# Optimization experiments

Measured on AMD Instinct MI355X. Metric: run time of the kernel, lower is better.

Reference implementation:

```python
import jax, jax.numpy as jnp
import numpy as np
import math

LOG2PI = math.log(2.0 * math.pi)
ALPHA, BETA, GAMMA = 1.0, 4.0, 1.0  # coefficients (mi, tc, dw_kl)


def gaussian_log_density(samples, mean, log_var):
    inv_sigma = jnp.exp(-log_var)
    tmp = samples - mean
    return -0.5 * (tmp * tmp * inv_sigma + log_var + LOG2PI)


def log_importance_weight_matrix(batch_size, dataset_size):
    # Faithful port of the TF/beta-tcvae MSS importance weights.
    N = float(dataset_size)
    M = batch_size - 1
    strat_weight = (N - M) / (N * M)
    W = jnp.full((batch_size, batch_size), 1.0 / M, dtype=jnp.float32)
    W = W.at[:, 0].set(1.0 / N)
    W = W.at[:, 1].set(strat_weight)
    W = W.at[M - 1, 0].set(strat_weight)
    return jnp.log(W)


def setup_inputs() -> dict:
    key = jax.random.key(0)
    k1, k2, k3, k4, k5 = jax.random.split(key, 5)
    B, D, F = 2048, 16, 512
    return {
        "x": jax.random.normal(k1, (B, F), dtype=jnp.float32),
        "reconstruction": jax.random.normal(k2, (B, F), dtype=jnp.float32),
        "mu": jax.random.normal(k3, (B, D), dtype=jnp.float32),
        "log_var": jax.random.normal(k4, (B, D), dtype=jnp.float32) * 0.5,
        "z": jax.random.normal(k5, (B, D), dtype=jnp.float32),
        "size_dataset": 100000,
    }


def reference(x, reconstruction, mu, log_var, z, size_dataset):
    B = z.shape[0]
    # reconstruction loss: mean over batch of per-sample MAE == global mean abs error
    recon_loss = jnp.mean(jnp.abs(x - reconstruction))

    # log q(z|x): [B]
    log_q_zx = jnp.sum(gaussian_log_density(z, mu, log_var), axis=-1)

    # pairwise densities: [B, B, D]  (z_i under q(.|x_j))
    log_qz_prob = gaussian_log_density(z[:, None, :], mu[None, :, :], log_var[None, :, :])

    # log p(z): note the original passes ones_like(z) as log_var (faithful quirk)
    log_prior = jnp.sum(
        gaussian_log_density(z, jnp.zeros_like(z), jnp.ones_like(z)), axis=-1
    )

    # MSS importance weights [B, B]
    logiw = log_importance_weight_matrix(B, size_dataset)

    # log q(z): logsumexp over batch of joint densities + weights
    log_qz = jax.nn.logsumexp(jnp.sum(log_qz_prob, axis=2) + logiw, axis=1)  # [B]

    # log prod_d q(z_d): dimension-wise logsumexp then sum over dims
    log_qz_product = jnp.sum(
        jax.nn.logsumexp(log_qz_prob + logiw[:, :, None], axis=1), axis=1
    )  # [B]

    mutual_info_loss = jnp.mean(log_q_zx - log_qz)
    tc_loss = jnp.mean(log_qz - log_qz_product)
    dimension_wise_kl = jnp.mean(log_qz_product - log_prior)

    total_loss = (
        recon_loss
        + ALPHA * mutual_info_loss
        + BETA * tc_loss
        + GAMMA * dimension_wise_kl
    )
    return total_loss
```

## Files before the change

### kernel.cpp

```cpp
#include <hip/hip_runtime.h>
#include <math.h>

#define LOG2PI_F 1.8378770664093453f
#define LOG2E_F  1.4426950408889634f
#define LN2_F    0.6931471805599453f
#define EXP_NEG1 0.36787944117144233f

#define TI   16
#define JSP  8
#define STG  64
#define ROWF 52

__device__ __forceinline__ float exp2_(float x) { return __builtin_amdgcn_exp2f(x); }
__device__ __forceinline__ float log2_(float x) { return __builtin_amdgcn_logf(x); }


__global__ __launch_bounds__(256) void k_recon(const float4* __restrict__ x,
                                               const float4* __restrict__ r,
                                               float* __restrict__ acc, int n4) {
    float s = 0.0f;
    for (int idx = blockIdx.x * 256 + threadIdx.x; idx < n4; idx += gridDim.x * 256) {
        float4 a = x[idx], b = r[idx];
        s += fabsf(a.x - b.x) + fabsf(a.y - b.y) + fabsf(a.z - b.z) + fabsf(a.w - b.w);
    }
    #pragma unroll
    for (int off = 32; off > 0; off >>= 1) s += __shfl_down(s, off);
    __shared__ float red[4];
    int lane = threadIdx.x & 63, wv = threadIdx.x >> 6;
    if (lane == 0) red[wv] = s;
    __syncthreads();
    if (threadIdx.x == 0) atomicAdd(&acc[0], red[0] + red[1] + red[2] + red[3]);
}

__global__ __launch_bounds__(256) void k_prep(const float* __restrict__ mu,
                                              const float* __restrict__ lv,
                                              const float* __restrict__ z,
                                              const int* __restrict__ nds,
                                              float* __restrict__ AC,
                                              float* __restrict__ acc, int B) {
    int idx = blockIdx.x * 256 + threadIdx.x;
    int j = idx >> 4, d = idx & 15;
    float m = mu[idx], l = lv[idx], zz = z[idx];
    float is = __expf(-l);
    float a = -0.5f * LOG2E_F * is;
    float b = -2.0f * a * m;
    float ec = fmaf(-0.5f * LOG2E_F, l + LOG2PI_F, a * m * m);

    float Nf = (float)(*nds);
    float Mf = (float)(B - 1);
    float strat = (Nf - Mf) / (Nf * Mf);
    float w = (j == 0) ? (1.0f / Nf) : ((j == 1) ? strat : (1.0f / Mf));

    float* row = AC + (size_t)j * ROWF;
    row[d] = a;
    row[16 + d] = b;
    row[32 + d] = w * exp2_(ec);
    float es = ec;
    es += __shfl_xor(es, 1); es += __shfl_xor(es, 2);
    es += __shfl_xor(es, 4); es += __shfl_xor(es, 8);
    if (d == 0) row[48] = w * exp2_(es);

    float t = zz - m;
    float ga = -0.5f * (fmaf(t * t, is, l) + LOG2PI_F);
    float gb = -0.5f * (fmaf(zz * zz, EXP_NEG1, 1.0f) + LOG2PI_F);
    #pragma unroll
    for (int off = 32; off > 0; off >>= 1) { ga += __shfl_down(ga, off); gb += __shfl_down(gb, off); }
    __shared__ float ra[4], rb[4];
    int lane = threadIdx.x & 63, wv = threadIdx.x >> 6;
    if (lane == 0) { ra[wv] = ga; rb[wv] = gb; }
    __syncthreads();
    if (threadIdx.x == 0) {
        atomicAdd(&acc[1], ra[0] + ra[1] + ra[2] + ra[3]);
        atomicAdd(&acc[2], rb[0] + rb[1] + rb[2] + rb[3]);
    }
}

#define DIM(AQ, BQ, CQ, comp, dd, SACC) \
    e = fmaf(AQ.comp, v2[dd], BQ.comp * v[dd]); SACC += e; \
    sd[dd] = fmaf(CQ.comp, exp2_(e), sd[dd]);

__global__ __launch_bounds__(256) void k_pair(const float* __restrict__ AC,
                                              const float* __restrict__ z,
                                              float* __restrict__ Racc,
                                              int B, int jch) {
    __shared__ float sbuf[2][STG * ROWF];
    __shared__ float red[4][TI][17];

    const int il = threadIdx.x & 15;
    const int jg = threadIdx.x >> 4;
    const int i  = blockIdx.x * TI + il;
    const int jbase = blockIdx.y * jch;

    float v[16], v2[16];
    {
        const float4* zp = (const float4*)(z + (size_t)i * 16);
        float4 z0 = zp[0], z1 = zp[1], z2 = zp[2], z3 = zp[3];
        v[0]=z0.x; v[1]=z0.y; v[2]=z0.z; v[3]=z0.w;
        v[4]=z1.x; v[5]=z1.y; v[6]=z1.z; v[7]=z1.w;
        v[8]=z2.x; v[9]=z2.y; v[10]=z2.z; v[11]=z2.w;
        v[12]=z3.x; v[13]=z3.y; v[14]=z3.z; v[15]=z3.w;
        #pragma unroll
        for (int d = 0; d < 16; d++) v2[d] = v[d] * v[d];
    }

    float sd[16];
    #pragma unroll
    for (int d = 0; d < 16; d++) sd[d] = 0.0f;
    float stot = 0.0f;

    auto load_stage = [&](int buf, int st) {
        const float4* g = (const float4*)(AC + (size_t)(jbase + st * STG) * ROWF);
        float4* dst = (float4*)sbuf[buf];
        #pragma unroll
        for (int k = 0; k < 4; ++k) {
            int idx = threadIdx.x + k * 256;
            if (idx < (STG * ROWF) / 4) dst[idx] = g[idx];
        }
    };

    const int nst = jch / STG;
    load_stage(0, 0);
    __syncthreads();
    for (int st = 0; st < nst; ++st) {
        if (st + 1 < nst) load_stage((st + 1) & 1, st + 1);
        const float* base = sbuf[st & 1];
        #pragma unroll
        for (int k = 0; k < 4; ++k) {
            const float* rp = base + (jg + 16 * k) * ROWF;
            const float4* r4 = (const float4*)rp;
            float4 A0 = r4[0], A1 = r4[1], A2 = r4[2], A3 = r4[3];
            float4 Bv0 = r4[4], Bv1 = r4[5], Bv2 = r4[6], Bv3 = r4[7];
            float4 Cv0 = r4[8], Cv1 = r4[9], Cv2 = r4[10], Cv3 = r4[11];
            float  P = rp[48];
            float s2a = 0.0f, s2b = 0.0f, e;
            DIM(A0, Bv0, Cv0, x, 0, s2a)  DIM(A0, Bv0, Cv0, y, 1, s2b)
            DIM(A0, Bv0, Cv0, z, 2, s2a)  DIM(A0, Bv0, Cv0, w, 3, s2b)
            DIM(A1, Bv1, Cv1, x, 4, s2a)  DIM(A1, Bv1, Cv1, y, 5, s2b)
            DIM(A1, Bv1, Cv1, z, 6, s2a)  DIM(A1, Bv1, Cv1, w, 7, s2b)
            DIM(A2, Bv2, Cv2, x, 8, s2a)  DIM(A2, Bv2, Cv2, y, 9, s2b)
            DIM(A2, Bv2, Cv2, z, 10, s2a) DIM(A2, Bv2, Cv2, w, 11, s2b)
            DIM(A3, Bv3, Cv3, x, 12, s2a) DIM(A3, Bv3, Cv3, y, 13, s2b)
            DIM(A3, Bv3, Cv3, z, 14, s2a) DIM(A3, Bv3, Cv3, w, 15, s2b)
            stot = fmaf(P, exp2_(s2a + s2b), stot);
        }
        __syncthreads();
    }

    #pragma unroll
    for (int msk = 16; msk <= 32; msk <<= 1) {
        stot += __shfl_xor(stot, msk);
        #pragma unroll
        for (int d = 0; d < 16; d++) sd[d] += __shfl_xor(sd[d], msk);
    }
    int lane = threadIdx.x & 63, wv = threadIdx.x >> 6;
    if (lane < 16) {
        red[wv][lane][0] = stot;
        #pragma unroll
        for (int d = 0; d < 16; d++) red[wv][lane][1 + d] = sd[d];
    }
    __syncthreads();
    for (int t = threadIdx.x; t < TI * 17; t += 256) {
        int il2 = t / 17, c = t % 17;
        float s = red[0][il2][c] + red[1][il2][c] + red[2][il2][c] + red[3][il2][c];
        atomicAdd(&Racc[(size_t)(blockIdx.x * TI + il2) * 17 + c], s);
    }
}

__global__ __launch_bounds__(256) void k_logs(const float* __restrict__ Racc,
                                              const float* __restrict__ AC,
                                              const float* __restrict__ z,
                                              const int* __restrict__ nds,
                                              float* __restrict__ acc, int B) {
    int i = blockIdx.x * 256 + threadIdx.x;
    const float* R = Racc + (size_t)i * 17;
    float S = R[0];
    float Sd[16];
    #pragma unroll
    for (int d = 0; d < 16; d++) Sd[d] = R[1 + d];

    if (i == B - 2) {
        const float* row0 = AC;
        const float* vv = z + (size_t)i * 16;
        float Nf = (float)(*nds);
        float Mf = (float)(B - 1);
        float strat = (Nf - Mf) / (Nf * Mf);
        float dwN = (strat - 1.0f / Nf) * Nf;
        float s2 = 0.0f;
        #pragma unroll
        for (int d = 0; d < 16; d++) {
            float vd = vv[d];
            float e = fmaf(row0[d], vd * vd, row0[16 + d] * vd);
            s2 += e;
            Sd[d] += dwN * row0[32 + d] * exp2_(e);
        }
        S += dwN * row0[48] * exp2_(s2);
    }

    float lqz = log2_(S) * LN2_F;
    float lqzp = 0.0f;
    #pragma unroll
    for (int d = 0; d < 16; d++) lqzp += log2_(Sd[d]);
    lqzp *= LN2_F;

    #pragma unroll
    for (int off = 32; off > 0; off >>= 1) {
        lqz += __shfl_down(lqz, off);
        lqzp += __shfl_down(lqzp, off);
    }
    __shared__ float ra[4], rb[4];
    int lane = threadIdx.x & 63, wv = threadIdx.x >> 6;
    if (lane == 0) { ra[wv] = lqz; rb[wv] = lqzp; }
    __syncthreads();
    if (threadIdx.x == 0) {
        atomicAdd(&acc[3], ra[0] + ra[1] + ra[2] + ra[3]);
        atomicAdd(&acc[4], rb[0] + rb[1] + rb[2] + rb[3]);
    }
}

__global__ void k_final(const float* __restrict__ acc, float* __restrict__ out,
                        float invBF, float invB) {
    out[0] = acc[0] * invBF +
             (acc[1] + 3.0f * acc[3] - 3.0f * acc[4] - acc[2]) * invB;
}

extern "C" void kernel_launch(void* const* d_in, const int* in_sizes, int n_in,
                              void* d_out, int out_size, void* d_ws, size_t ws_size,
                              hipStream_t stream) {
    const float* x   = (const float*)d_in[0];
    const float* rec = (const float*)d_in[1];
    const float* mu  = (const float*)d_in[2];
    const float* lv  = (const float*)d_in[3];
    const float* z   = (const float*)d_in[4];
    const int*   nds = (const int*)d_in[5];

    const int BD = in_sizes[2];
    const int B  = BD / 16;
    const int BF = in_sizes[0];
    const int n4 = BF / 4;

    float* acc  = (float*)d_ws;
    float* Racc = acc + 8;
    float* AC   = Racc + (size_t)B * 17;

    hipMemsetAsync(d_ws, 0, (8 + (size_t)B * 17) * sizeof(float), stream);
    k_prep <<<BD / 256, 256, 0, stream>>>(mu, lv, z, nds, AC, acc, B);
    k_recon<<<512, 256, 0, stream>>>((const float4*)x, (const float4*)rec, acc, n4);
    dim3 gp(B / TI, JSP);
    k_pair <<<gp, 256, 0, stream>>>(AC, z, Racc, B, B / JSP);
    k_logs <<<B / 256, 256, 0, stream>>>(Racc, AC, z, nds, acc, B);
    k_final<<<1, 1, 0, stream>>>(acc, (float*)d_out, 1.0f / (float)BF, 1.0f / (float)B);
}
```

Measured before the change: 100.1 us.

## Fuse prep and recon kernels, register-block two rows per thread, drop atomics and memset

Merges the prep and reconstruction-loss kernels into one launch. Partial sums now go to per-block slots reduced by a multi-thread final kernel, which replaces the atomics and removes the workspace memset. The pair kernel now handles two z rows per thread (TI 32, JSP 16) so each shared-memory load of the coefficients is reused twice. It also loads its whole 128-row j chunk into shared memory once instead of double-buffering. The intent is fewer launches, less atomic contention and more ALU work per LDS read, at the cost of higher register pressure and a larger strided partial-sum buffer.

```diff
diff --git a/kernel.cpp b/kernel.cpp
--- a/kernel.cpp
+++ b/kernel.cpp
@@ -6,177 +6,192 @@
 #define LN2_F    0.6931471805599453f
 #define EXP_NEG1 0.36787944117144233f
 
-#define TI   16
-#define JSP  8
-#define STG  64
+#define TI   32
+#define JSP  16
+#define JCH  128
 #define ROWF 52
 
 __device__ __forceinline__ float exp2_(float x) { return __builtin_amdgcn_exp2f(x); }
 __device__ __forceinline__ float log2_(float x) { return __builtin_amdgcn_logf(x); }
 
 
-__global__ __launch_bounds__(256) void k_recon(const float4* __restrict__ x,
-                                               const float4* __restrict__ r,
-                                               float* __restrict__ acc, int n4) {
-    float s = 0.0f;
-    for (int idx = blockIdx.x * 256 + threadIdx.x; idx < n4; idx += gridDim.x * 256) {
-        float4 a = x[idx], b = r[idx];
-        s += fabsf(a.x - b.x) + fabsf(a.y - b.y) + fabsf(a.z - b.z) + fabsf(a.w - b.w);
-    }
-    #pragma unroll
-    for (int off = 32; off > 0; off >>= 1) s += __shfl_down(s, off);
-    __shared__ float red[4];
-    int lane = threadIdx.x & 63, wv = threadIdx.x >> 6;
-    if (lane == 0) red[wv] = s;
-    __syncthreads();
-    if (threadIdx.x == 0) atomicAdd(&acc[0], red[0] + red[1] + red[2] + red[3]);
-}
-
-__global__ __launch_bounds__(256) void k_prep(const float* __restrict__ mu,
-                                              const float* __restrict__ lv,
-                                              const float* __restrict__ z,
-                                              const int* __restrict__ nds,
-                                              float* __restrict__ AC,
-                                              float* __restrict__ acc, int B) {
-    int idx = blockIdx.x * 256 + threadIdx.x;
-    int j = idx >> 4, d = idx & 15;
-    float m = mu[idx], l = lv[idx], zz = z[idx];
-    float is = __expf(-l);
-    float a = -0.5f * LOG2E_F * is;
-    float b = -2.0f * a * m;
-    float ec = fmaf(-0.5f * LOG2E_F, l + LOG2PI_F, a * m * m);
-
-    float Nf = (float)(*nds);
-    float Mf = (float)(B - 1);
-    float strat = (Nf - Mf) / (Nf * Mf);
-    float w = (j == 0) ? (1.0f / Nf) : ((j == 1) ? strat : (1.0f / Mf));
-
-    float* row = AC + (size_t)j * ROWF;
-    row[d] = a;
-    row[16 + d] = b;
-    row[32 + d] = w * exp2_(ec);
-    float es = ec;
-    es += __shfl_xor(es, 1); es += __shfl_xor(es, 2);
-    es += __shfl_xor(es, 4); es += __shfl_xor(es, 8);
-    if (d == 0) row[48] = w * exp2_(es);
-
-    float t = zz - m;
-    float ga = -0.5f * (fmaf(t * t, is, l) + LOG2PI_F);
-    float gb = -0.5f * (fmaf(zz * zz, EXP_NEG1, 1.0f) + LOG2PI_F);
-    #pragma unroll
-    for (int off = 32; off > 0; off >>= 1) { ga += __shfl_down(ga, off); gb += __shfl_down(gb, off); }
+__global__ __launch_bounds__(256) void k_prep_recon(
+        const float* __restrict__ mu, const float* __restrict__ lv,
+        const float* __restrict__ z, const int* __restrict__ nds,
+        const float4* __restrict__ x, const float4* __restrict__ r,
+        float* __restrict__ AC, float* __restrict__ PPa, float* __restrict__ PPb,
+        float* __restrict__ RP, int B, int n4, int prepBlks) {
     __shared__ float ra[4], rb[4];
-    int lane = threadIdx.x & 63, wv = threadIdx.x >> 6;
-    if (lane == 0) { ra[wv] = ga; rb[wv] = gb; }
-    __syncthreads();
-    if (threadIdx.x == 0) {
-        atomicAdd(&acc[1], ra[0] + ra[1] + ra[2] + ra[3]);
-        atomicAdd(&acc[2], rb[0] + rb[1] + rb[2] + rb[3]);
-    }
-}
-
-#define DIM(AQ, BQ, CQ, comp, dd, SACC) \
-    e = fmaf(AQ.comp, v2[dd], BQ.comp * v[dd]); SACC += e; \
-    sd[dd] = fmaf(CQ.comp, exp2_(e), sd[dd]);
+    const int lane = threadIdx.x & 63, wv = threadIdx.x >> 6;
+
+    if ((int)blockIdx.x < prepBlks) {
+        int idx = blockIdx.x * 256 + threadIdx.x;
+        int j = idx >> 4, d = idx & 15;
+        float m = mu[idx], l = lv[idx], zz = z[idx];
+        float is = __expf(-l);
+        float a = -0.5f * LOG2E_F * is;
+        float b = -2.0f * a * m;
+        float ec = fmaf(-0.5f * LOG2E_F, l + LOG2PI_F, a * m * m);
+
+        float Nf = (float)(*nds);
+        float Mf = (float)(B - 1);
+        float strat = (Nf - Mf) / (Nf * Mf);
+        float w = (j == 0) ? (1.0f / Nf) : ((j == 1) ? strat : (1.0f / Mf));
+
+        float* row = AC + (size_t)j * ROWF;
+        row[d] = a;
+        row[16 + d] = b;
+        row[32 + d] = w * exp2_(ec);
+        float es = ec;
+        es += __shfl_xor(es, 1); es += __shfl_xor(es, 2);
+        es += __shfl_xor(es, 4); es += __shfl_xor(es, 8);
+        if (d == 0) row[48] = w * exp2_(es);
+
+        float t = zz - m;
+        float ga = -0.5f * (fmaf(t * t, is, l) + LOG2PI_F);
+        float gb = -0.5f * (fmaf(zz * zz, EXP_NEG1, 1.0f) + LOG2PI_F);
+        #pragma unroll
+        for (int off = 32; off > 0; off >>= 1) { ga += __shfl_down(ga, off); gb += __shfl_down(gb, off); }
+        if (lane == 0) { ra[wv] = ga; rb[wv] = gb; }
+        __syncthreads();
+        if (threadIdx.x == 0) {
+            PPa[blockIdx.x] = ra[0] + ra[1] + ra[2] + ra[3];
+            PPb[blockIdx.x] = rb[0] + rb[1] + rb[2] + rb[3];
+        }
+    } else {
+        int bid = blockIdx.x - prepBlks;
+        float s = 0.0f;
+        for (int idx = bid * 256 + threadIdx.x; idx < n4; idx += 512 * 256) {
+            float4 a = x[idx], b = r[idx];
+            s += fabsf(a.x - b.x) + fabsf(a.y - b.y) + fabsf(a.z - b.z) + fabsf(a.w - b.w);
+        }
+        #pragma unroll
+        for (int off = 32; off > 0; off >>= 1) s += __shfl_down(s, off);
+        if (lane == 0) ra[wv] = s;
+        __syncthreads();
+        if (threadIdx.x == 0) RP[bid] = ra[0] + ra[1] + ra[2] + ra[3];
+    }
+}
+
+#define DIM2(AQ, BQ, CQ, comp, dd, SA, SB) \
+    e = fmaf(AQ.comp, va2[dd], BQ.comp * va[dd]); SA += e; sda[dd] = fmaf(CQ.comp, exp2_(e), sda[dd]); \
+    e = fmaf(AQ.comp, vb2[dd], BQ.comp * vb[dd]); SB += e; sdb[dd] = fmaf(CQ.comp, exp2_(e), sdb[dd]);
 
 __global__ __launch_bounds__(256) void k_pair(const float* __restrict__ AC,
                                               const float* __restrict__ z,
-                                              float* __restrict__ Racc,
+                                              float* __restrict__ Rs,
                                               int B, int jch) {
-    __shared__ float sbuf[2][STG * ROWF];
+    __shared__ float sbuf[JCH * ROWF];
     __shared__ float red[4][TI][17];
 
     const int il = threadIdx.x & 15;
     const int jg = threadIdx.x >> 4;
-    const int i  = blockIdx.x * TI + il;
+    const int i0 = blockIdx.x * TI + il;
     const int jbase = blockIdx.y * jch;
 
-    float v[16], v2[16];
     {
-        const float4* zp = (const float4*)(z + (size_t)i * 16);
+        const float4* g = (const float4*)(AC + (size_t)jbase * ROWF);
+        float4* dst = (float4*)sbuf;
+        #pragma unroll
+        for (int k = 0; k < 7; ++k) {
+            int idx = threadIdx.x + k * 256;
+            if (idx < (JCH * ROWF) / 4) dst[idx] = g[idx];
+        }
+    }
+
+    float va[16], va2[16], vb[16], vb2[16];
+    {
+        const float4* zp = (const float4*)(z + (size_t)i0 * 16);
         float4 z0 = zp[0], z1 = zp[1], z2 = zp[2], z3 = zp[3];
-        v[0]=z0.x; v[1]=z0.y; v[2]=z0.z; v[3]=z0.w;
-        v[4]=z1.x; v[5]=z1.y; v[6]=z1.z; v[7]=z1.w;
-        v[8]=z2.x; v[9]=z2.y; v[10]=z2.z; v[11]=z2.w;
-        v[12]=z3.x; v[13]=z3.y; v[14]=z3.z; v[15]=z3.w;
-        #pragma unroll
-        for (int d = 0; d < 16; d++) v2[d] = v[d] * v[d];
-    }
-
-    float sd[16];
-    #pragma unroll
-    for (int d = 0; d < 16; d++) sd[d] = 0.0f;
-    float stot = 0.0f;
-
-    auto load_stage = [&](int buf, int st) {
-        const float4* g = (const float4*)(AC + (size_t)(jbase + st * STG) * ROWF);
-        float4* dst = (float4*)sbuf[buf];
-        #pragma unroll
-        for (int k = 0; k < 4; ++k) {
-            int idx = threadIdx.x + k * 256;
-            if (idx < (STG * ROWF) / 4) dst[idx] = g[idx];
-        }
-    };
-
-    const int nst = jch / STG;
-    load_stage(0, 0);
-    __syncthreads();
-    for (int st = 0; st < nst; ++st) {
-        if (st + 1 < nst) load_stage((st + 1) & 1, st + 1);
-        const float* base = sbuf[st & 1];
-        #pragma unroll
-        for (int k = 0; k < 4; ++k) {
-            const float* rp = base + (jg + 16 * k) * ROWF;
-            const float4* r4 = (const float4*)rp;
-            float4 A0 = r4[0], A1 = r4[1], A2 = r4[2], A3 = r4[3];
-            float4 Bv0 = r4[4], Bv1 = r4[5], Bv2 = r4[6], Bv3 = r4[7];
-            float4 Cv0 = r4[8], Cv1 = r4[9], Cv2 = r4[10], Cv3 = r4[11];
-            float  P = rp[48];
-            float s2a = 0.0f, s2b = 0.0f, e;
-            DIM(A0, Bv0, Cv0, x, 0, s2a)  DIM(A0, Bv0, Cv0, y, 1, s2b)
-            DIM(A0, Bv0, Cv0, z, 2, s2a)  DIM(A0, Bv0, Cv0, w, 3, s2b)
-            DIM(A1, Bv1, Cv1, x, 4, s2a)  DIM(A1, Bv1, Cv1, y, 5, s2b)
-            DIM(A1, Bv1, Cv1, z, 6, s2a)  DIM(A1, Bv1, Cv1, w, 7, s2b)
-            DIM(A2, Bv2, Cv2, x, 8, s2a)  DIM(A2, Bv2, Cv2, y, 9, s2b)
-            DIM(A2, Bv2, Cv2, z, 10, s2a) DIM(A2, Bv2, Cv2, w, 11, s2b)
-            DIM(A3, Bv3, Cv3, x, 12, s2a) DIM(A3, Bv3, Cv3, y, 13, s2b)
-            DIM(A3, Bv3, Cv3, z, 14, s2a) DIM(A3, Bv3, Cv3, w, 15, s2b)
-            stot = fmaf(P, exp2_(s2a + s2b), stot);
-        }
-        __syncthreads();
+        va[0]=z0.x; va[1]=z0.y; va[2]=z0.z; va[3]=z0.w;
+        va[4]=z1.x; va[5]=z1.y; va[6]=z1.z; va[7]=z1.w;
+        va[8]=z2.x; va[9]=z2.y; va[10]=z2.z; va[11]=z2.w;
+        va[12]=z3.x; va[13]=z3.y; va[14]=z3.z; va[15]=z3.w;
+        const float4* zq = (const float4*)(z + (size_t)(i0 + 16) * 16);
+        float4 y0 = zq[0], y1 = zq[1], y2 = zq[2], y3 = zq[3];
+        vb[0]=y0.x; vb[1]=y0.y; vb[2]=y0.z; vb[3]=y0.w;
+        vb[4]=y1.x; vb[5]=y1.y; vb[6]=y1.z; vb[7]=y1.w;
+        vb[8]=y2.x; vb[9]=y2.y; vb[10]=y2.z; vb[11]=y2.w;
+        vb[12]=y3.x; vb[13]=y3.y; vb[14]=y3.z; vb[15]=y3.w;
+        #pragma unroll
+        for (int d = 0; d < 16; d++) { va2[d] = va[d] * va[d]; vb2[d] = vb[d] * vb[d]; }
+    }
+
+    float sda[16], sdb[16];
+    #pragma unroll
+    for (int d = 0; d < 16; d++) { sda[d] = 0.0f; sdb[d] = 0.0f; }
+    float stA = 0.0f, stB = 0.0f;
+
+    __syncthreads();
+
+    const int nk = jch >> 4;
+    for (int k = 0; k < nk; ++k) {
+        const float* rp = sbuf + (jg + 16 * k) * ROWF;
+        const float4* r4 = (const float4*)rp;
+        float sa0 = 0.0f, sa1 = 0.0f, sb0 = 0.0f, sb1 = 0.0f, e;
+        {
+            float4 A0 = r4[0], A1 = r4[1], Bq0 = r4[4], Bq1 = r4[5], C0 = r4[8], C1 = r4[9];
+            DIM2(A0, Bq0, C0, x, 0, sa0, sb0)  DIM2(A0, Bq0, C0, y, 1, sa1, sb1)
+            DIM2(A0, Bq0, C0, z, 2, sa0, sb0)  DIM2(A0, Bq0, C0, w, 3, sa1, sb1)
+            DIM2(A1, Bq1, C1, x, 4, sa0, sb0)  DIM2(A1, Bq1, C1, y, 5, sa1, sb1)
+            DIM2(A1, Bq1, C1, z, 6, sa0, sb0)  DIM2(A1, Bq1, C1, w, 7, sa1, sb1)
+        }
+        {
+            float4 A2 = r4[2], A3 = r4[3], Bq2 = r4[6], Bq3 = r4[7], C2 = r4[10], C3 = r4[11];
+            DIM2(A2, Bq2, C2, x, 8, sa0, sb0)  DIM2(A2, Bq2, C2, y, 9, sa1, sb1)
+            DIM2(A2, Bq2, C2, z, 10, sa0, sb0) DIM2(A2, Bq2, C2, w, 11, sa1, sb1)
+            DIM2(A3, Bq3, C3, x, 12, sa0, sb0) DIM2(A3, Bq3, C3, y, 13, sa1, sb1)
+            DIM2(A3, Bq3, C3, z, 14, sa0, sb0) DIM2(A3, Bq3, C3, w, 15, sa1, sb1)
+        }
+        float P = rp[48];
+        stA = fmaf(P, exp2_(sa0 + sa1), stA);
+        stB = fmaf(P, exp2_(sb0 + sb1), stB);
     }
 
     #pragma unroll
     for (int msk = 16; msk <= 32; msk <<= 1) {
-        stot += __shfl_xor(stot, msk);
-        #pragma unroll
-        for (int d = 0; d < 16; d++) sd[d] += __shfl_xor(sd[d], msk);
-    }
-    int lane = threadIdx.x & 63, wv = threadIdx.x >> 6;
+        stA += __shfl_xor(stA, msk);
+        stB += __shfl_xor(stB, msk);
+        #pragma unroll
+        for (int d = 0; d < 16; d++) {
+            sda[d] += __shfl_xor(sda[d], msk);
+            sdb[d] += __shfl_xor(sdb[d], msk);
+        }
+    }
+    const int lane = threadIdx.x & 63, wv = threadIdx.x >> 6;
     if (lane < 16) {
-        red[wv][lane][0] = stot;
-        #pragma unroll
-        for (int d = 0; d < 16; d++) red[wv][lane][1 + d] = sd[d];
+        red[wv][lane][0] = stA;
+        red[wv][lane + 16][0] = stB;
+        #pragma unroll
+        for (int d = 0; d < 16; d++) {
+            red[wv][lane][1 + d] = sda[d];
+            red[wv][lane + 16][1 + d] = sdb[d];
+        }
     }
     __syncthreads();
     for (int t = threadIdx.x; t < TI * 17; t += 256) {
-        int il2 = t / 17, c = t % 17;
+        int il2 = t & 31, c = t >> 5;
         float s = red[0][il2][c] + red[1][il2][c] + red[2][il2][c] + red[3][il2][c];
-        atomicAdd(&Racc[(size_t)(blockIdx.x * TI + il2) * 17 + c], s);
-    }
-}
-
-__global__ __launch_bounds__(256) void k_logs(const float* __restrict__ Racc,
+        Rs[((size_t)blockIdx.y * 17 + c) * B + blockIdx.x * TI + il2] = s;
+    }
+}
+
+__global__ __launch_bounds__(256) void k_logs(const float* __restrict__ Rs,
                                               const float* __restrict__ AC,
                                               const float* __restrict__ z,
                                               const int* __restrict__ nds,
-                                              float* __restrict__ acc, int B) {
+                                              float* __restrict__ LPa,
+                                              float* __restrict__ LPb, int B) {
     int i = blockIdx.x * 256 + threadIdx.x;
-    const float* R = Racc + (size_t)i * 17;
-    float S = R[0];
-    float Sd[16];
-    #pragma unroll
-    for (int d = 0; d < 16; d++) Sd[d] = R[1 + d];
+    float S = 0.0f, Sd[16];
+    #pragma unroll
+    for (int d = 0; d < 16; d++) Sd[d] = 0.0f;
+    for (int sp = 0; sp < JSP; ++sp) {
+        const float* base = Rs + (size_t)sp * 17 * B + i;
+        S += base[0];
+        #pragma unroll
+        for (int d = 0; d < 16; d++) Sd[d] += base[(size_t)(1 + d) * B];
+    }
 
     if (i == B - 2) {
         const float* row0 = AC;
@@ -212,15 +227,41 @@
     if (lane == 0) { ra[wv] = lqz; rb[wv] = lqzp; }
     __syncthreads();
     if (threadIdx.x == 0) {
-        atomicAdd(&acc[3], ra[0] + ra[1] + ra[2] + ra[3]);
-        atomicAdd(&acc[4], rb[0] + rb[1] + rb[2] + rb[3]);
-    }
-}
-
-__global__ void k_final(const float* __restrict__ acc, float* __restrict__ out,
-                        float invBF, float invB) {
-    out[0] = acc[0] * invBF +
-             (acc[1] + 3.0f * acc[3] - 3.0f * acc[4] - acc[2]) * invB;
+        LPa[blockIdx.x] = ra[0] + ra[1] + ra[2] + ra[3];
+        LPb[blockIdx.x] = rb[0] + rb[1] + rb[2] + rb[3];
+    }
+}
+
+__global__ void k_final(const float* __restrict__ RP, const float* __restrict__ PPa,
+                        const float* __restrict__ PPb, const float* __restrict__ LPa,
+                        const float* __restrict__ LPb, float* __restrict__ out,
+                        float invBF, float invB, int prepBlks, int logBlks) {
+    int tid = threadIdx.x;
+    float sr = 0.0f, sga = 0.0f, sgb = 0.0f, slz = 0.0f, slp = 0.0f;
+    for (int t = tid; t < 512; t += 256) sr += RP[t];
+    for (int t = tid; t < prepBlks; t += 256) { sga += PPa[t]; sgb += PPb[t]; }
+    for (int t = tid; t < logBlks; t += 256) { slz += LPa[t]; slp += LPb[t]; }
+    #pragma unroll
+    for (int off = 32; off > 0; off >>= 1) {
+        sr += __shfl_down(sr, off);   sga += __shfl_down(sga, off);
+        sgb += __shfl_down(sgb, off); slz += __shfl_down(slz, off);
+        slp += __shfl_down(slp, off);
+    }
+    __shared__ float red[4][5];
+    int lane = tid & 63, wv = tid >> 6;
+    if (lane == 0) {
+        red[wv][0] = sr; red[wv][1] = sga; red[wv][2] = sgb;
+        red[wv][3] = slz; red[wv][4] = slp;
+    }
+    __syncthreads();
+    if (tid == 0) {
+        float R  = red[0][0] + red[1][0] + red[2][0] + red[3][0];
+        float GA = red[0][1] + red[1][1] + red[2][1] + red[3][1];
+        float GB = red[0][2] + red[1][2] + red[2][2] + red[3][2];
+        float LZ = red[0][3] + red[1][3] + red[2][3] + red[3][3];
+        float LQ = red[0][4] + red[1][4] + red[2][4] + red[3][4];
+        out[0] = R * invBF + (GA + 3.0f * LZ - 3.0f * LQ - GB) * invB;
+    }
 }
 
 extern "C" void kernel_launch(void* const* d_in, const int* in_sizes, int n_in,
@@ -237,16 +278,22 @@
     const int B  = BD / 16;
     const int BF = in_sizes[0];
     const int n4 = BF / 4;
-
-    float* acc  = (float*)d_ws;
-    float* Racc = acc + 8;
-    float* AC   = Racc + (size_t)B * 17;
-
-    hipMemsetAsync(d_ws, 0, (8 + (size_t)B * 17) * sizeof(float), stream);
-    k_prep <<<BD / 256, 256, 0, stream>>>(mu, lv, z, nds, AC, acc, B);
-    k_recon<<<512, 256, 0, stream>>>((const float4*)x, (const float4*)rec, acc, n4);
+    const int prepBlks = BD / 256;
+    const int logBlks  = B / 256;
+
+    float* AC  = (float*)d_ws;
+    float* Rs  = AC + (size_t)B * 52;
+    float* PPa = Rs + (size_t)JSP * 17 * B;
+    float* PPb = PPa + prepBlks;
+    float* RP  = PPb + prepBlks;
+    float* LPa = RP + 512;
+    float* LPb = LPa + logBlks;
+
+    k_prep_recon<<<prepBlks + 512, 256, 0, stream>>>(mu, lv, z, nds,
+        (const float4*)x, (const float4*)rec, AC, PPa, PPb, RP, B, n4, prepBlks);
     dim3 gp(B / TI, JSP);
-    k_pair <<<gp, 256, 0, stream>>>(AC, z, Racc, B, B / JSP);
-    k_logs <<<B / 256, 256, 0, stream>>>(Racc, AC, z, nds, acc, B);
-    k_final<<<1, 1, 0, stream>>>(acc, (float*)d_out, 1.0f / (float)BF, 1.0f / (float)B);
-}
+    k_pair <<<gp, 256, 0, stream>>>(AC, z, Rs, B, B / JSP);
+    k_logs <<<logBlks, 256, 0, stream>>>(Rs, AC, z, nds, LPa, LPb, B);
+    k_final<<<1, 256, 0, stream>>>(RP, PPa, PPb, LPa, LPb, (float*)d_out,
+                                   1.0f / (float)BF, 1.0f / (float)B, prepBlks, logBlks);
+}
```

After: 93.80 us. -6.3%, faster.
